# Kernel tuning notes

Measured on AMD Instinct MI355X. Metric: run time of the kernel, lower is better.

The kernel has to match this reference:

```python
import jax, jax.numpy as jnp
import numpy as np
import math

G0, G1 = 24, 24           # initial/current grid size (command(initial_grid_size=(24,24), ...))
N = G0 * G1               # 576 spatial tokens
PREFIX = 1                # num_prefix_tokens (cls token)
EPS = 0.1                 # get_eps((24,24)): 0.5*23^2/0.1^2 = 26450 <= 32500, no doubling
COEF = float(max(G0, G1) ** 2)          # 576.0, sigmoid_fn coefficient
B_SHIFT = math.log(COEF - 1.0)          # b = log(575)
CLAMP = max(-0.5 * (max(G0, G1) - 1) ** 2, -6550.0)  # -264.5


def setup_inputs() -> dict:
    key = jax.random.key(0)
    k1, k2, k3 = jax.random.split(key, 3)
    head_dim = 64
    q = jax.random.normal(k1, (8, 12, N + PREFIX, head_dim), dtype=jnp.float32)
    W_var = jax.random.normal(k2, (head_dim, 2), dtype=jnp.float32) * (head_dim ** -0.5)
    b_var = jnp.zeros((2,), dtype=jnp.float32)
    W_alpha = jax.random.normal(k3, (head_dim, 1), dtype=jnp.float32) * (head_dim ** -0.5)
    b_alpha = jnp.zeros((1,), dtype=jnp.float32)
    return {"q": q, "W_var": W_var, "b_var": b_var, "W_alpha": W_alpha, "b_alpha": b_alpha}


def _gaussian_numerator():
    # coords: (N, 2) integer grid positions
    ii, jj = jnp.meshgrid(jnp.arange(G0), jnp.arange(G1), indexing="ij")
    coords = jnp.stack([ii, jj], axis=-1).reshape(N, 2).astype(jnp.float32)
    d = -0.5 * (coords[:, None, :] - coords[None, :, :]) ** 2  # (N, N, 2)
    return jnp.maximum(d, CLAMP)


def reference(q, W_var, b_var, W_alpha, b_alpha):
    qs = q[..., PREFIX:, :]                                   # (B, H, N, C)
    # var = coef * sigmoid(linear(q) - b), shape (B, H, N, 2)
    var = COEF * jax.nn.sigmoid(jnp.einsum("bhnc,ck->bhnk", qs, W_var) + b_var - B_SHIFT)
    # alpha = softplus(linear(q)), shape (B, H, N, 1)
    alpha = jax.nn.softplus(jnp.einsum("bhnc,ck->bhnk", qs, W_alpha) + b_alpha)
    d = _gaussian_numerator()                                 # (N, N, 2)
    # broadcast divide -> sum over coord dim -> exp: (B, H, N, N)
    gaussian = jnp.exp(jnp.sum(d[None, None] / (var[:, :, :, None, :] + EPS), axis=-1))
    addition = alpha * gaussian                               # alpha broadcasts over last dim
    # pad prefix rows/cols with 0 at the beginning -> (B, H, N+1, N+1)
    return jnp.pad(addition, ((0, 0), (0, 0), (PREFIX, 0), (PREFIX, 0)))
```

## Files before the change

### kernel.cpp

```cpp
#include <hip/hip_runtime.h>
#include <math.h>

#define G 24
#define NPTS (G * G)
#define ROWS (NPTS + 1)
#define HD 64
#define BH (8 * 12)
#define EPSF 0.1f
#define COEFF 576.0f
#define BSHIFT 6.3543700408f
#define RPB 16
#define BPI ((ROWS + RPB - 1) / RPB)

typedef float f32x4 __attribute__((ext_vector_type(4)));

__global__ __launch_bounds__(256) void gaussian_augment_kernel(
    const float* __restrict__ q,
    const float* __restrict__ Wv,
    const float* __restrict__ bv,
    const float* __restrict__ Wa,
    const float* __restrict__ ba,
    float* __restrict__ out)
{
    const int bh  = blockIdx.x / BPI;
    const int blk = blockIdx.x - bh * BPI;
    const int r0  = blk * RPB;
    const int Ract = min(RPB, ROWS - r0);
    const int tid = threadIdx.x;

    __shared__ float s_part[RPB][16][3];
    __shared__ float s_par[RPB][4];
    __shared__ float s_tab[RPB][2][32];

    {
        const int r  = tid >> 4;
        const int kk = tid & 15;
        float p0 = 0.f, p1 = 0.f, p2 = 0.f;
        if (r < Ract) {
            const float* qp = q + ((size_t)bh * ROWS + r0 + r) * HD + 4 * kk;
            const f32x4 qv = *(const f32x4*)qp;
            const f32x4 wv0 = *(const f32x4*)(Wv + 8 * kk);
            const f32x4 wv1 = *(const f32x4*)(Wv + 8 * kk + 4);
            const f32x4 wav = *(const f32x4*)(Wa + 4 * kk);
            p0 = qv[0]*wv0[0] + qv[1]*wv0[2] + qv[2]*wv1[0] + qv[3]*wv1[2];
            p1 = qv[0]*wv0[1] + qv[1]*wv0[3] + qv[2]*wv1[1] + qv[3]*wv1[3];
            p2 = qv[0]*wav[0] + qv[1]*wav[1] + qv[2]*wav[2] + qv[3]*wav[3];
        }
        s_part[r][kk][0] = p0;
        s_part[r][kk][1] = p1;
        s_part[r][kk][2] = p2;
    }
    __syncthreads();

    if (tid < 3 * RPB) {
        const int pr = tid / 3;
        const int pp = tid - 3 * pr;
        if (pr < Ract) {
            float x = 0.f;
            #pragma unroll
            for (int k = 0; k < 16; ++k) x += s_part[pr][k][pp];
            float o;
            if (pp == 2) {
                const float xa = x + ba[0];
                float al = fmaxf(xa, 0.f) + log1pf(expf(-fabsf(xa)));
                if (r0 + pr == 0) al = 0.f;
                o = al;
            } else {
                const float xx = x + bv[pp] - BSHIFT;
                const float var = COEFF / (1.f + expf(-xx));
                o = 1.f / (var + EPSF);
            }
            s_par[pr][pp] = o;
        }
    }
    __syncthreads();

    for (int e = tid; e < 49 * Ract; e += 256) {
        const int rr = (unsigned)e / 49u;
        const int k  = e - 49 * rr;
        const int rg = r0 + rr;
        const int n  = (rg > 0) ? rg - 1 : 0;
        const int in_ = (unsigned)n / 24u;
        const int jn_ = n - in_ * 24;
        if (k < 25) {
            const float t = (float)(in_ - k);
            s_tab[rr][0][k] = s_par[rr][2] * expf(-0.5f * t * t * s_par[rr][0]);
        } else {
            const float t = (float)(jn_ - (k - 25));
            s_tab[rr][1][k - 25] = expf(-0.5f * t * t * s_par[rr][1]);
        }
    }
    __syncthreads();

    const size_t base = ((size_t)bh * ROWS + r0) * ROWS;
    const int span  = Ract * ROWS;
    const size_t S0 = base & ~(size_t)3;
    const int   off = (int)(base - S0);
    const int   nch = (span + off + 3) >> 2;

    for (int idx = tid; idx < nch; idx += 256) {
        const int eb = 4 * idx - off;
        const size_t g0 = S0 + (size_t)4 * idx;
        if (eb >= 0 && eb + 4 <= span) {
            float v0, v1, v2, v3;
            const unsigned eu = (unsigned)eb;
            const int rr = (int)(eu / 577u);
            const int c0 = eb - rr * 577;
            if (c0 >= 1 && c0 <= 573) {
                const int m0  = c0 - 1;
                const int im0 = (unsigned)m0 / 24u;
                const int jm0 = m0 - im0 * 24;
                const float ea = s_tab[rr][0][im0];
                const float eb2 = s_tab[rr][0][im0 + 1];
                const float* t1 = s_tab[rr][1];
                {
                    const int j = jm0;     const bool w = j >= 24;
                    v0 = (w ? eb2 : ea) * t1[w ? j - 24 : j];
                }
                {
                    const int j = jm0 + 1; const bool w = j >= 24;
                    v1 = (w ? eb2 : ea) * t1[w ? j - 24 : j];
                }
                {
                    const int j = jm0 + 2; const bool w = j >= 24;
                    v2 = (w ? eb2 : ea) * t1[w ? j - 24 : j];
                }
                {
                    const int j = jm0 + 3; const bool w = j >= 24;
                    v3 = (w ? eb2 : ea) * t1[w ? j - 24 : j];
                }
            } else {
                float vv[4];
                #pragma unroll
                for (int t = 0; t < 4; ++t) {
                    const int e = eb + t;
                    const unsigned eu2 = (unsigned)e;
                    const int r2 = (int)(eu2 / 577u);
                    const int c  = e - r2 * 577;
                    float val = 0.f;
                    if (c > 0) {
                        const unsigned m = (unsigned)(c - 1);
                        const int im = (int)(m / 24u);
                        const int jm = (int)m - im * 24;
                        val = s_tab[r2][0][im] * s_tab[r2][1][jm];
                    }
                    vv[t] = val;
                }
                v0 = vv[0]; v1 = vv[1]; v2 = vv[2]; v3 = vv[3];
            }
            f32x4 pk = { v0, v1, v2, v3 };
            __builtin_nontemporal_store(pk, (f32x4*)(out + g0));
        } else {
            #pragma unroll
            for (int t = 0; t < 4; ++t) {
                const int e = eb + t;
                if (e >= 0 && e < span) {
                    const unsigned eu2 = (unsigned)e;
                    const int r2 = (int)(eu2 / 577u);
                    const int c  = e - r2 * 577;
                    float val = 0.f;
                    if (c > 0) {
                        const unsigned m = (unsigned)(c - 1);
                        const int im = (int)(m / 24u);
                        const int jm = (int)m - im * 24;
                        val = s_tab[r2][0][im] * s_tab[r2][1][jm];
                    }
                    out[g0 + t] = val;
                }
            }
        }
    }
}

extern "C" void kernel_launch(void* const* d_in, const int* in_sizes, int n_in,
                              void* d_out, int out_size, void* d_ws, size_t ws_size,
                              hipStream_t stream) {
    const float* q  = (const float*)d_in[0];
    const float* Wv = (const float*)d_in[1];
    const float* bv = (const float*)d_in[2];
    const float* Wa = (const float*)d_in[3];
    const float* ba = (const float*)d_in[4];
    float* out = (float*)d_out;

    const int grid = BH * BPI;
    gaussian_augment_kernel<<<grid, 256, 0, stream>>>(q, Wv, bv, Wa, ba, out);
}
```

Measured before the change: 40.87 us.

## Map threads per row with float4 stores from separable exponent tables

Replaces the flat chunked store loop, which divides by 577 and takes boundary branches, with a per-row mapping. Each of 16 threads per row writes 9 float4 stores, each the product of one row-factor scalar and a float4 slice of the column-factor table. The prefix column is written separately by one thread per row, and the shared tables are split and aligned so they can be read as float4. The aim is to cut integer-division and branch overhead in this store-bound kernel. The cost is that the global float4 stores now start at row base + 1, so they are generally not 16-byte aligned.

```diff
diff --git a/kernel.cpp b/kernel.cpp
--- a/kernel.cpp
+++ b/kernel.cpp
@@ -30,7 +30,8 @@
 
     __shared__ float s_part[RPB][16][3];
     __shared__ float s_par[RPB][4];
-    __shared__ float s_tab[RPB][2][32];
+    __shared__ __align__(16) float s_ex0[RPB][32];
+    __shared__ __align__(16) float s_ex1[RPB][32];
 
     {
         const int r  = tid >> 4;
@@ -38,7 +39,7 @@
         float p0 = 0.f, p1 = 0.f, p2 = 0.f;
         if (r < Ract) {
             const float* qp = q + ((size_t)bh * ROWS + r0 + r) * HD + 4 * kk;
-            const f32x4 qv = *(const f32x4*)qp;
+            const f32x4 qv  = *(const f32x4*)qp;
             const f32x4 wv0 = *(const f32x4*)(Wv + 8 * kk);
             const f32x4 wv1 = *(const f32x4*)(Wv + 8 * kk + 4);
             const f32x4 wav = *(const f32x4*)(Wa + 4 * kk);
@@ -75,98 +76,47 @@
     }
     __syncthreads();
 
-    for (int e = tid; e < 49 * Ract; e += 256) {
-        const int rr = (unsigned)e / 49u;
-        const int k  = e - 49 * rr;
+    for (int e = tid; e < 48 * Ract; e += 256) {
+        const int rr = (int)((unsigned)e / 48u);
+        const int k  = e - 48 * rr;
         const int rg = r0 + rr;
         const int n  = (rg > 0) ? rg - 1 : 0;
-        const int in_ = (unsigned)n / 24u;
+        const int in_ = (int)((unsigned)n / 24u);
         const int jn_ = n - in_ * 24;
-        if (k < 25) {
+        if (k < 24) {
             const float t = (float)(in_ - k);
-            s_tab[rr][0][k] = s_par[rr][2] * expf(-0.5f * t * t * s_par[rr][0]);
+            s_ex0[rr][k] = s_par[rr][2] * expf(-0.5f * t * t * s_par[rr][0]);
         } else {
-            const float t = (float)(jn_ - (k - 25));
-            s_tab[rr][1][k - 25] = expf(-0.5f * t * t * s_par[rr][1]);
+            const float t = (float)(jn_ - (k - 24));
+            s_ex1[rr][k - 24] = expf(-0.5f * t * t * s_par[rr][1]);
         }
     }
     __syncthreads();
 
-    const size_t base = ((size_t)bh * ROWS + r0) * ROWS;
-    const int span  = Ract * ROWS;
-    const size_t S0 = base & ~(size_t)3;
-    const int   off = (int)(base - S0);
-    const int   nch = (span + off + 3) >> 2;
+    if (tid < Ract) {
+        out[((size_t)bh * ROWS + r0 + tid) * ROWS] = 0.0f;
+    }
 
-    for (int idx = tid; idx < nch; idx += 256) {
-        const int eb = 4 * idx - off;
-        const size_t g0 = S0 + (size_t)4 * idx;
-        if (eb >= 0 && eb + 4 <= span) {
-            float v0, v1, v2, v3;
-            const unsigned eu = (unsigned)eb;
-            const int rr = (int)(eu / 577u);
-            const int c0 = eb - rr * 577;
-            if (c0 >= 1 && c0 <= 573) {
-                const int m0  = c0 - 1;
-                const int im0 = (unsigned)m0 / 24u;
-                const int jm0 = m0 - im0 * 24;
-                const float ea = s_tab[rr][0][im0];
-                const float eb2 = s_tab[rr][0][im0 + 1];
-                const float* t1 = s_tab[rr][1];
-                {
-                    const int j = jm0;     const bool w = j >= 24;
-                    v0 = (w ? eb2 : ea) * t1[w ? j - 24 : j];
-                }
-                {
-                    const int j = jm0 + 1; const bool w = j >= 24;
-                    v1 = (w ? eb2 : ea) * t1[w ? j - 24 : j];
-                }
-                {
-                    const int j = jm0 + 2; const bool w = j >= 24;
-                    v2 = (w ? eb2 : ea) * t1[w ? j - 24 : j];
-                }
-                {
-                    const int j = jm0 + 3; const bool w = j >= 24;
-                    v3 = (w ? eb2 : ea) * t1[w ? j - 24 : j];
-                }
-            } else {
-                float vv[4];
-                #pragma unroll
-                for (int t = 0; t < 4; ++t) {
-                    const int e = eb + t;
-                    const unsigned eu2 = (unsigned)e;
-                    const int r2 = (int)(eu2 / 577u);
-                    const int c  = e - r2 * 577;
-                    float val = 0.f;
-                    if (c > 0) {
-                        const unsigned m = (unsigned)(c - 1);
-                        const int im = (int)(m / 24u);
-                        const int jm = (int)m - im * 24;
-                        val = s_tab[r2][0][im] * s_tab[r2][1][jm];
-                    }
-                    vv[t] = val;
-                }
-                v0 = vv[0]; v1 = vv[1]; v2 = vv[2]; v3 = vv[3];
-            }
-            f32x4 pk = { v0, v1, v2, v3 };
-            __builtin_nontemporal_store(pk, (f32x4*)(out + g0));
-        } else {
+    {
+        const int r = tid >> 4;
+        const int l = tid & 15;
+        if (r < Ract) {
+            float* rowp = out + ((size_t)bh * ROWS + r0 + r) * ROWS + 1;
+            const float* e0p = s_ex0[r];
+            const float* e1p = s_ex1[r];
             #pragma unroll
-            for (int t = 0; t < 4; ++t) {
-                const int e = eb + t;
-                if (e >= 0 && e < span) {
-                    const unsigned eu2 = (unsigned)e;
-                    const int r2 = (int)(eu2 / 577u);
-                    const int c  = e - r2 * 577;
-                    float val = 0.f;
-                    if (c > 0) {
-                        const unsigned m = (unsigned)(c - 1);
-                        const int im = (int)(m / 24u);
-                        const int jm = (int)m - im * 24;
-                        val = s_tab[r2][0][im] * s_tab[r2][1][jm];
-                    }
-                    out[g0 + t] = val;
-                }
+            for (int it = 0; it < 9; ++it) {
+                const int k  = l + 16 * it;
+                const int im = (int)((unsigned)k / 6u);
+                const int u  = k - 6 * im;
+                const float  e0 = e0p[im];
+                const f32x4  e1 = *(const f32x4*)(e1p + 4 * u);
+                f32x4 pk;
+                pk[0] = e0 * e1[0];
+                pk[1] = e0 * e1[1];
+                pk[2] = e0 * e1[2];
+                pk[3] = e0 * e1[3];
+                __builtin_nontemporal_store(pk, (f32x4*)(rowp + 4 * k));
             }
         }
     }
```

Result: slower. 45.51 us (+11.3%).
